# Kernel tuning notes

Measured on AMD Instinct MI355X. Metric: run time of the kernel, lower is better.

Reference implementation:

```python
import jax, jax.numpy as jnp
import numpy as np

B, S, D = 4, 4096, 256

def setup_inputs() -> dict:
    key = jax.random.key(0)
    ks = jax.random.split(key, 9)
    sc = 1.0 / np.sqrt(D)
    return {
        "v": jax.random.normal(ks[0], (B, S, D), jnp.float32),
        "k": jax.random.normal(ks[1], (B, S, D), jnp.float32),
        "q": jax.random.normal(ks[2], (B, S, D), jnp.float32),
        "Wq": jax.random.normal(ks[3], (D, D), jnp.float32) * sc,
        "bq": jnp.zeros((D,), jnp.float32),
        "Wk": jax.random.normal(ks[4], (D, D), jnp.float32) * sc,
        "bk": jnp.zeros((D,), jnp.float32),
        "Wv": jax.random.normal(ks[5], (D, D), jnp.float32) * sc,
        "bv": jnp.zeros((D,), jnp.float32),
    }

def reference(v, k, q, Wq, bq, Wk, bk, Wv, bv):
    d_model = q.shape[-1]
    seq_len = q.shape[-2]
    qp = q @ Wq + bq                      # [B,S,D]
    kp = k @ Wk + bk
    vp = v @ Wv + bv
    # scores [B,S,S], scaled then MULTIPLIED by lower-triangular mask (faithful to original)
    scores = jnp.einsum('bqd,bkd->bqk', qp, kp) / jnp.sqrt(jnp.float32(d_model))
    mask = jnp.tril(jnp.ones((seq_len, seq_len), scores.dtype))
    scores = scores * mask
    attn = jax.nn.softmax(scores, axis=-1)
    return qp + jnp.einsum('bqk,bkd->bqd', attn, vp)
```

## Files before the change

kernel.cpp:

```cpp
#include <hip/hip_runtime.h>
#include <hip/hip_bf16.h>


typedef __bf16 bf16x8 __attribute__((ext_vector_type(8)));
typedef float f32x4 __attribute__((ext_vector_type(4)));
typedef float f32x16 __attribute__((ext_vector_type(16)));
typedef unsigned int u32x4 __attribute__((ext_vector_type(4)));

#define MASKV -3.0e38f

__device__ __forceinline__ unsigned short f2bf_u(float f) {
  unsigned u = __float_as_uint(f);
  u += 0x7fffu + ((u >> 16) & 1u);
  return (unsigned short)(u >> 16);
}
__device__ __forceinline__ float bf2f(unsigned u16) {
  return __uint_as_float(u16 << 16);
}
__device__ __forceinline__ unsigned short cvt_bf(float f) {
  return __builtin_bit_cast(unsigned short, (__bf16)f);
}

__global__ __launch_bounds__(256) void wt_kernel(
    const float* __restrict__ Wq, const float* __restrict__ Wk, const float* __restrict__ Wv,
    unsigned short* __restrict__ WTq, unsigned short* __restrict__ WTk, unsigned short* __restrict__ WTv) {
  int j = blockIdx.x & 255;
  int wsel = blockIdx.x >> 8;
  const float* W = wsel == 0 ? Wq : (wsel == 1 ? Wk : Wv);
  unsigned short* WT = wsel == 0 ? WTq : (wsel == 1 ? WTk : WTv);
  int k = threadIdx.x;
  WT[j * 256 + k] = f2bf_u(W[k * 256 + j]);
}

__global__ __launch_bounds__(256) void proj_all_kernel(
    const float* __restrict__ q_in, const float* __restrict__ k_in, const float* __restrict__ v_in,
    const unsigned short* __restrict__ WTq, const unsigned short* __restrict__ WTk,
    const unsigned short* __restrict__ WTv,
    const float* __restrict__ bq, const float* __restrict__ bk, const float* __restrict__ bv,
    unsigned short* __restrict__ qpb, unsigned short* __restrict__ kpb,
    unsigned short* __restrict__ vptb) {
  int mode = blockIdx.y;
  const float* X = mode == 0 ? q_in : (mode == 1 ? k_in : v_in);
  const unsigned short* WT = mode == 0 ? WTq : (mode == 1 ? WTk : WTv);
  const float* bias = mode == 0 ? bq : (mode == 1 ? bk : bv);

  int rt = blockIdx.x;
  int tid = threadIdx.x;
  int w = tid >> 6, l = tid & 63, g = l >> 4, lm = l & 15;
  int arow = rt * 64 + w * 16 + lm;

  f32x4 acc[16];
#pragma unroll
  for (int i = 0; i < 16; i++) acc[i] = (f32x4){0.f, 0.f, 0.f, 0.f};

#pragma unroll
  for (int kb = 0; kb < 256; kb += 32) {
    const float* ap = X + arow * 256 + kb + 8 * g;
    float4 a0 = *(const float4*)ap;
    float4 a1 = *(const float4*)(ap + 4);
    bf16x8 af;
    af[0] = (__bf16)a0.x; af[1] = (__bf16)a0.y; af[2] = (__bf16)a0.z; af[3] = (__bf16)a0.w;
    af[4] = (__bf16)a1.x; af[5] = (__bf16)a1.y; af[6] = (__bf16)a1.z; af[7] = (__bf16)a1.w;
#pragma unroll
    for (int nt = 0; nt < 16; nt++) {
      bf16x8 bf = *(const bf16x8*)(WT + (nt * 16 + lm) * 256 + kb + 8 * g);
      acc[nt] = __builtin_amdgcn_mfma_f32_16x16x32_bf16(af, bf, acc[nt], 0, 0, 0);
    }
  }

#pragma unroll
  for (int nt = 0; nt < 16; nt++) {
    int col = nt * 16 + lm;
    float bb = bias[col];
#pragma unroll
    for (int r = 0; r < 4; r++) {
      int orow = rt * 64 + w * 16 + 4 * g + r;
      float v = acc[nt][r] + bb;
      int idx = orow * 256 + col;
      if (mode == 0) {
        qpb[idx] = f2bf_u(v * 0.0625f);
      } else if (mode == 1) {
        kpb[idx] = f2bf_u(v * 1.4426950408889634f);
      } else {
        int b = orow >> 12, sidx = orow & 4095;
        vptb[(((size_t)b * 128 + (sidx >> 5)) * 256 + col) * 32 + (sidx & 31)] = f2bf_u(v);
      }
    }
  }
}

__global__ __launch_bounds__(256) void scan1(const unsigned short* __restrict__ vptb,
                                             float* __restrict__ ctot) {
  int c = blockIdx.x, b = blockIdx.y, d = threadIdx.x;
  const unsigned short* base = vptb + (((size_t)b * 128 + c) * 256 + d) * 32;
  float acc = 0.f;
#pragma unroll
  for (int r = 0; r < 32; r++) acc += bf2f(base[r]);
  ctot[(b * 128 + c) * 256 + d] = acc;
}

__global__ __launch_bounds__(256) void scan2(const unsigned short* __restrict__ vptb,
                                             const float* __restrict__ ctot,
                                             unsigned short* __restrict__ suffv) {
  int c = blockIdx.x, b = blockIdx.y, d = threadIdx.x;
  float acc = 0.f;
  for (int c2 = c + 1; c2 < 128; c2++) acc += ctot[(b * 128 + c2) * 256 + d];
  const unsigned short* base = vptb + (((size_t)b * 128 + c) * 256 + d) * 32;
  unsigned short* sbase = suffv + ((size_t)b * 4096 + c * 32) * 256 + d;
  for (int r = 31; r >= 0; r--) {
    sbase[r * 256] = f2bf_u(acc);
    acc += bf2f(base[r]);
  }
}

__global__ __launch_bounds__(256, 2) void attn13_kernel(
    const unsigned short* __restrict__ qpb, const unsigned short* __restrict__ kpb,
    const unsigned short* __restrict__ vptb,
    unsigned short* __restrict__ slot01,
    unsigned short* __restrict__ slot23,
    unsigned short* __restrict__ slot45,
    float* __restrict__ mz) {
  extern __shared__ char smem[];

  int bid = blockIdx.x;
  int low = bid & 7;
  int b = low >> 1, shi = low & 1;
  int j = bid >> 3;
  int jd3 = j / 3;
  int qb = 31 - jd3;
  int s = shi * 3 + (j - jd3 * 3);
  int NT = 4 * (qb + 1);
  int t0 = (s * NT) / 6, t1 = ((s + 1) * NT) / 6;

  int tid = threadIdx.x;
  int wv = tid >> 6, l = tid & 63;
  int hi = l >> 5, r32 = l & 31;
  int vsw = (r32 >> 1) & 3;
  int ksw = r32 & 7;

  int qwave = qb * 128 + 32 * wv;
  int qglob = qwave + r32;

  bf16x8 qf[16];
  const unsigned short* qsrc = qpb + (size_t)(b * 4096 + qwave + r32) * 256;
#pragma unroll
  for (int st = 0; st < 16; st++) qf[st] = *(const bf16x8*)(qsrc + st * 16 + 8 * hi);

  f32x16 zero16;
#pragma unroll
  for (int ee = 0; ee < 16; ee++) zero16[ee] = 0.f;
  f32x16 O[8];
#pragma unroll
  for (int dt = 0; dt < 8; dt++) O[dt] = zero16;
  float m_ = -1e30f, Z_ = 0.f;

  const unsigned short* kbase0 = kpb + (size_t)b * 4096 * 256;
  const unsigned short* vbase0 = vptb + (size_t)b * 128 * 256 * 32;

  auto STAGE = [&](int bi, int kt) {
    char* Kdst = smem + bi * 16384;
    char* Vdst = smem + 32768 + bi * 16384;
    const unsigned short* ksrc = kbase0 + (size_t)kt * 32 * 256;
    const unsigned short* vtile = vbase0 + (size_t)kt * 256 * 32;
#pragma unroll
    for (int j2 = 0; j2 < 4; j2++) {
      int ch = wv * 4 + j2;
      int row = ch * 2 + (l >> 5);
      int cc = (l & 31) ^ (row & 7);
      __builtin_amdgcn_global_load_lds(
          (const __attribute__((address_space(1))) unsigned int*)(ksrc + row * 256 + cc * 8),
          (__attribute__((address_space(3))) unsigned int*)(Kdst + ch * 1024), 16, 0, 0);
    }
#pragma unroll
    for (int j2 = 0; j2 < 4; j2++) {
      int ch = wv * 4 + j2;
      int d = ch * 16 + (l >> 2);
      int cc = (l & 3) ^ ((l >> 3) & 3);
      __builtin_amdgcn_global_load_lds(
          (const __attribute__((address_space(1))) unsigned int*)(vtile + d * 32 + cc * 8),
          (__attribute__((address_space(3))) unsigned int*)(Vdst + ch * 1024), 16, 0, 0);
    }
  };

  if (t0 < t1) {
    STAGE(0, t0);
    if (t0 + 1 < t1) STAGE(1, t0 + 1);
  }

  for (int kt = t0; kt < t1; kt++) {
    int cur = (kt - t0) & 1;
    int kb2 = kt * 32;

    if (kt + 1 < t1) asm volatile("s_waitcnt vmcnt(8)" ::: "memory");
    else             asm volatile("s_waitcnt vmcnt(0)" ::: "memory");
    __builtin_amdgcn_s_barrier();
    __builtin_amdgcn_sched_barrier(0);

    if (kb2 <= qwave + 31) {
      const char* Kp = smem + cur * 16384;
      const char* Vp = smem + 32768 + cur * 16384;

      f32x16 St;
      __builtin_amdgcn_s_setprio(1);
      {
        bf16x8 kf = *(const bf16x8*)(Kp + r32 * 512 + ((hi ^ ksw) * 16));
        St = __builtin_amdgcn_mfma_f32_32x32x16_bf16(kf, qf[0], zero16, 0, 0, 0);
      }
#pragma unroll
      for (int st = 1; st < 16; st++) {
        bf16x8 kf = *(const bf16x8*)(Kp + r32 * 512 + (((2 * st + hi) ^ ksw) * 16));
        St = __builtin_amdgcn_mfma_f32_32x32x16_bf16(kf, qf[st], St, 0, 0, 0);
      }
      __builtin_amdgcn_s_setprio(0);

      if (kb2 + 31 > qwave) {
#pragma unroll
        for (int r = 0; r < 16; r++) {
          int kg = kb2 + (r & 3) + 8 * (r >> 2) + 4 * hi;
          if (kg > qglob) St[r] = MASKV;
        }
      }

      float mx = fmaxf(fmaxf(fmaxf(St[0], St[1]), fmaxf(St[2], St[3])),
                       fmaxf(fmaxf(St[4], St[5]), fmaxf(St[6], St[7])));
      float mx2 = fmaxf(fmaxf(fmaxf(St[8], St[9]), fmaxf(St[10], St[11])),
                        fmaxf(fmaxf(St[12], St[13]), fmaxf(St[14], St[15])));
      mx = fmaxf(mx, mx2);
      mx = fmaxf(mx, __shfl_xor(mx, 32));
      bool upd = __any(mx > m_ + 8.f);
      if (upd) {
        float mn = fmaxf(m_, mx);
        float scl = exp2f(m_ - mn);
        m_ = mn;
        Z_ *= scl;
#pragma unroll
        for (int r = 0; r < 16; r++) {
          int qr = (r & 3) + 8 * (r >> 2) + 4 * hi;
          float sb = __uint_as_float(
              (unsigned)__builtin_amdgcn_ds_bpermute(qr * 4, (int)__float_as_uint(scl)));
#pragma unroll
          for (int dt = 0; dt < 8; dt++) O[dt][r] *= sb;
        }
      }
      float p[16];
#pragma unroll
      for (int r = 0; r < 16; r++) p[r] = exp2f(St[r] - m_);
      float rs = ((p[0] + p[1]) + (p[2] + p[3])) + ((p[4] + p[5]) + (p[6] + p[7])) +
                 (((p[8] + p[9]) + (p[10] + p[11])) + ((p[12] + p[13]) + (p[14] + p[15])));
      rs += __shfl_xor(rs, 32);
      Z_ += rs;

      unsigned X[8];
#pragma unroll
      for (int i = 0; i < 8; i++)
        X[i] = (unsigned)cvt_bf(p[2 * i]) | ((unsigned)cvt_bf(p[2 * i + 1]) << 16);
      unsigned Y0 = (unsigned)__shfl_xor((int)X[0], 32);
      unsigned Y1 = (unsigned)__shfl_xor((int)X[1], 32);
      unsigned Y2 = (unsigned)__shfl_xor((int)X[2], 32);
      unsigned Y3 = (unsigned)__shfl_xor((int)X[3], 32);
      unsigned Y4 = (unsigned)__shfl_xor((int)X[4], 32);
      unsigned Y5 = (unsigned)__shfl_xor((int)X[5], 32);
      unsigned Y6 = (unsigned)__shfl_xor((int)X[6], 32);
      unsigned Y7 = (unsigned)__shfl_xor((int)X[7], 32);
      u32x4 A0, A1;
      A0[0] = hi ? Y2 : X[0]; A0[1] = hi ? Y3 : X[1];
      A0[2] = hi ? X[2] : Y0; A0[3] = hi ? X[3] : Y1;
      A1[0] = hi ? Y6 : X[4]; A1[1] = hi ? Y7 : X[5];
      A1[2] = hi ? X[6] : Y4; A1[3] = hi ? X[7] : Y5;
      bf16x8 pa0 = __builtin_bit_cast(bf16x8, A0);
      bf16x8 pa1 = __builtin_bit_cast(bf16x8, A1);

      __builtin_amdgcn_s_setprio(1);
#pragma unroll
      for (int dt = 0; dt < 8; dt++) {
        bf16x8 vf0 = *(const bf16x8*)(Vp + (dt * 32 + r32) * 64 + ((hi ^ vsw) * 16));
        O[dt] = __builtin_amdgcn_mfma_f32_32x32x16_bf16(pa0, vf0, O[dt], 0, 0, 0);
      }
#pragma unroll
      for (int dt = 0; dt < 8; dt++) {
        bf16x8 vf1 = *(const bf16x8*)(Vp + (dt * 32 + r32) * 64 + (((2 + hi) ^ vsw) * 16));
        O[dt] = __builtin_amdgcn_mfma_f32_32x32x16_bf16(pa1, vf1, O[dt], 0, 0, 0);
      }
      __builtin_amdgcn_s_setprio(0);
    }

    __builtin_amdgcn_sched_barrier(0);
    __builtin_amdgcn_s_barrier();
    if (kt + 2 < t1) STAGE(cur, kt + 2);
  }

  int grow_base = b * 4096 + qwave;
  if (hi == 0) {
    float* mzm = mz + s * 32768;
    mzm[grow_base + r32] = m_;
    mzm[16384 + grow_base + r32] = Z_;
  }
#pragma unroll
  for (int r = 0; r < 16; r++) {
    int qr = (r & 3) + 8 * (r >> 2) + 4 * hi;
    size_t grow = (size_t)(grow_base + qr);
#pragma unroll
    for (int dt = 0; dt < 8; dt++) {
      int dcol = dt * 32 + r32;
      unsigned short vb = cvt_bf(O[dt][r]);
      if (s < 2)
        slot01[grow * 512 + (size_t)s * 256 + dcol] = vb;
      else if (s < 4)
        slot23[(size_t)(s - 2) * 4194304 + grow * 256 + dcol] = vb;
      else
        slot45[(size_t)(s - 4) * 4194304 + grow * 256 + dcol] = vb;
    }
  }
}

__global__ __launch_bounds__(256) void combine6_kernel(
    const float* __restrict__ mz,
    const unsigned short* __restrict__ slot23, const unsigned short* __restrict__ slot45,
    const unsigned short* __restrict__ qpb, const unsigned short* __restrict__ suffv,
    float* __restrict__ out) {
  int grow = blockIdx.x * 4 + (threadIdx.x >> 6);
  int col = (threadIdx.x & 63) * 4;
  const unsigned short* slot01 = (const unsigned short*)out;

  float mv[6], Zv[6];
#pragma unroll
  for (int s = 0; s < 6; s++) {
    const float* mzm = mz + s * 32768;
    mv[s] = mzm[grow];
    Zv[s] = mzm[16384 + grow];
  }
  float M = mv[0];
#pragma unroll
  for (int s = 1; s < 6; s++) M = fmaxf(M, mv[s]);
  float fs[6], Zm = 0.f;
#pragma unroll
  for (int s = 0; s < 6; s++) {
    fs[s] = exp2f(mv[s] - M);
    Zm += Zv[s] * fs[s];
  }

  int q = grow & 4095;
  int nmask = 4095 - q;
  float scl, e0, Zf;
  if (nmask > 0) {
    float Mf = fmaxf(M, 0.f);
    scl = exp2f(M - Mf);
    e0 = exp2f(-Mf);
    Zf = Zm * scl + (float)nmask * e0;
  } else {
    scl = 1.f; e0 = 0.f; Zf = Zm;
  }
  float rZ = 1.f / Zf;
  float a[6];
#pragma unroll
  for (int s = 0; s < 6; s++) a[s] = fs[s] * scl * rZ;
  float asv = e0 * rZ;

  size_t base = (size_t)grow * 256 + col;
  uint2 ss[6];
  ss[0] = *(const uint2*)(slot01 + (size_t)grow * 512 + col);
  ss[1] = *(const uint2*)(slot01 + (size_t)grow * 512 + 256 + col);
  ss[2] = *(const uint2*)(slot23 + base);
  ss[3] = *(const uint2*)(slot23 + 4194304 + base);
  ss[4] = *(const uint2*)(slot45 + base);
  ss[5] = *(const uint2*)(slot45 + 4194304 + base);
  uint2 qpr = *(const uint2*)(qpb + base);
  uint2 svu = *(const uint2*)(suffv + base);

  __syncthreads();

  float4 res;
  res.x = 16.f * bf2f(qpr.x & 0xffff) + bf2f(svu.x & 0xffff) * asv;
  res.y = 16.f * bf2f(qpr.x >> 16) + bf2f(svu.x >> 16) * asv;
  res.z = 16.f * bf2f(qpr.y & 0xffff) + bf2f(svu.y & 0xffff) * asv;
  res.w = 16.f * bf2f(qpr.y >> 16) + bf2f(svu.y >> 16) * asv;
#pragma unroll
  for (int s = 0; s < 6; s++) {
    res.x += bf2f(ss[s].x & 0xffff) * a[s];
    res.y += bf2f(ss[s].x >> 16) * a[s];
    res.z += bf2f(ss[s].y & 0xffff) * a[s];
    res.w += bf2f(ss[s].y >> 16) * a[s];
  }
  *(float4*)&out[base] = res;
}

extern "C" void kernel_launch(void* const* d_in, const int* in_sizes, int n_in,
                              void* d_out, int out_size, void* d_ws, size_t ws_size,
                              hipStream_t stream) {
  const float* v_in = (const float*)d_in[0];
  const float* k_in = (const float*)d_in[1];
  const float* q_in = (const float*)d_in[2];
  const float* Wq = (const float*)d_in[3];
  const float* bq = (const float*)d_in[4];
  const float* Wk = (const float*)d_in[5];
  const float* bk = (const float*)d_in[6];
  const float* Wv = (const float*)d_in[7];
  const float* bv = (const float*)d_in[8];
  float* out = (float*)d_out;

  char* p = (char*)d_ws;
  unsigned short* slot45 = (unsigned short*)(p + 0);
  unsigned short* slot23 = (unsigned short*)(p + 16777216);
  unsigned short* suffv = (unsigned short*)(p + 33554432);
  unsigned short* qpb = (unsigned short*)(p + 41943040);
  unsigned short* kpb = (unsigned short*)(p + 50331648);
  unsigned short* vptb = (unsigned short*)(p + 58720256);
  float* mz = (float*)(p + 67108864);
  unsigned short* WTq = (unsigned short*)(p + 67895296);
  unsigned short* WTk = (unsigned short*)(p + 68026368);
  unsigned short* WTv = (unsigned short*)(p + 68157440);
  float* ctot = (float*)(p + 68288512);
  unsigned short* slot01 = (unsigned short*)d_out;

  hipFuncSetAttribute((const void*)attn13_kernel,
                      hipFuncAttributeMaxDynamicSharedMemorySize, 65536);

  wt_kernel<<<768, 256, 0, stream>>>(Wq, Wk, Wv, WTq, WTk, WTv);
  proj_all_kernel<<<dim3(256, 3), 256, 0, stream>>>(q_in, k_in, v_in, WTq, WTk, WTv,
                                                    bq, bk, bv, qpb, kpb, vptb);
  scan1<<<dim3(128, 4), 256, 0, stream>>>(vptb, ctot);
  scan2<<<dim3(128, 4), 256, 0, stream>>>(vptb, ctot, suffv);
  attn13_kernel<<<768, 256, 65536, stream>>>(qpb, kpb, vptb, slot01, slot23, slot45, mz);
  combine6_kernel<<<4096, 256, 0, stream>>>(mz, slot23, slot45, qpb, suffv, out);
}
```

Before: 187.3 us.

## Stage projection weight tiles into LDS with async double-buffered global_load_lds

The projection GEMM used to read bf16 weight fragments straight from global memory inside the MFMA loop. It now copies each 32-wide K slice of the transposed weights into a double-buffered 32KB shared-memory region using global_load_lds, with an XOR swizzle to avoid bank conflicts. vmcnt waits and barriers overlap the next slice's load with the current MFMAs. This adds block-wide barriers and LDS use per block, and the projection is only a small part of the total pipeline. The attention kernel is only renamed.

Measured after the change: 151.8 us. 18.9% less time.

```diff
diff --git a/kernel.cpp b/kernel.cpp
--- a/kernel.cpp
+++ b/kernel.cpp
@@ -39,6 +39,8 @@
     const float* __restrict__ bq, const float* __restrict__ bk, const float* __restrict__ bv,
     unsigned short* __restrict__ qpb, unsigned short* __restrict__ kpb,
     unsigned short* __restrict__ vptb) {
+  __shared__ char bsmem[32768];
+
   int mode = blockIdx.y;
   const float* X = mode == 0 ? q_in : (mode == 1 ? k_in : v_in);
   const unsigned short* WT = mode == 0 ? WTq : (mode == 1 ? WTk : WTv);
@@ -48,24 +50,56 @@
   int tid = threadIdx.x;
   int w = tid >> 6, l = tid & 63, g = l >> 4, lm = l & 15;
   int arow = rt * 64 + w * 16 + lm;
+  int lsw = lm & 3;
 
   f32x4 acc[16];
 #pragma unroll
   for (int i = 0; i < 16; i++) acc[i] = (f32x4){0.f, 0.f, 0.f, 0.f};
 
-#pragma unroll
-  for (int kb = 0; kb < 256; kb += 32) {
+  auto BSTAGE = [&](int bi, int kb) {
+    char* dstbase = bsmem + bi * 16384 + w * 1024;
+#pragma unroll
+    for (int i = 0; i < 4; i++) {
+      int chunkid = i * 256 + w * 64 + l;
+      int col = chunkid >> 2, cc = chunkid & 3;
+      const unsigned short* src = WT + col * 256 + kb + 8 * (cc ^ (col & 3));
+      __builtin_amdgcn_global_load_lds(
+          (const __attribute__((address_space(1))) unsigned int*)src,
+          (__attribute__((address_space(3))) unsigned int*)(dstbase + i * 4096), 16, 0, 0);
+    }
+  };
+
+  BSTAGE(0, 0);
+  BSTAGE(1, 32);
+
+  for (int kb8 = 0; kb8 < 8; kb8++) {
+    int cur = kb8 & 1;
+    int kb = kb8 * 32;
+
+    if (kb8 + 1 < 8) asm volatile("s_waitcnt vmcnt(4)" ::: "memory");
+    else             asm volatile("s_waitcnt vmcnt(0)" ::: "memory");
+    __builtin_amdgcn_s_barrier();
+    __builtin_amdgcn_sched_barrier(0);
+
     const float* ap = X + arow * 256 + kb + 8 * g;
     float4 a0 = *(const float4*)ap;
     float4 a1 = *(const float4*)(ap + 4);
     bf16x8 af;
     af[0] = (__bf16)a0.x; af[1] = (__bf16)a0.y; af[2] = (__bf16)a0.z; af[3] = (__bf16)a0.w;
     af[4] = (__bf16)a1.x; af[5] = (__bf16)a1.y; af[6] = (__bf16)a1.z; af[7] = (__bf16)a1.w;
+
+    const char* Bs = bsmem + cur * 16384;
+    __builtin_amdgcn_s_setprio(1);
 #pragma unroll
     for (int nt = 0; nt < 16; nt++) {
-      bf16x8 bf = *(const bf16x8*)(WT + (nt * 16 + lm) * 256 + kb + 8 * g);
+      bf16x8 bf = *(const bf16x8*)(Bs + (nt * 16 + lm) * 64 + ((g ^ lsw) * 16));
       acc[nt] = __builtin_amdgcn_mfma_f32_16x16x32_bf16(af, bf, acc[nt], 0, 0, 0);
     }
+    __builtin_amdgcn_s_setprio(0);
+
+    __builtin_amdgcn_sched_barrier(0);
+    __builtin_amdgcn_s_barrier();
+    if (kb8 + 2 < 8) BSTAGE(cur, kb + 64);
   }
 
 #pragma unroll
@@ -113,7 +147,7 @@
   }
 }
 
-__global__ __launch_bounds__(256, 2) void attn13_kernel(
+__global__ __launch_bounds__(256, 2) void attn14_kernel(
     const unsigned short* __restrict__ qpb, const unsigned short* __restrict__ kpb,
     const unsigned short* __restrict__ vptb,
     unsigned short* __restrict__ slot01,
@@ -412,7 +446,7 @@
   float* ctot = (float*)(p + 68288512);
   unsigned short* slot01 = (unsigned short*)d_out;
 
-  hipFuncSetAttribute((const void*)attn13_kernel,
+  hipFuncSetAttribute((const void*)attn14_kernel,
                       hipFuncAttributeMaxDynamicSharedMemorySize, 65536);
 
   wt_kernel<<<768, 256, 0, stream>>>(Wq, Wk, Wv, WTq, WTk, WTv);
@@ -420,6 +454,6 @@
                                                     bq, bk, bv, qpb, kpb, vptb);
   scan1<<<dim3(128, 4), 256, 0, stream>>>(vptb, ctot);
   scan2<<<dim3(128, 4), 256, 0, stream>>>(vptb, ctot, suffv);
-  attn13_kernel<<<768, 256, 65536, stream>>>(qpb, kpb, vptb, slot01, slot23, slot45, mz);
+  attn14_kernel<<<768, 256, 65536, stream>>>(qpb, kpb, vptb, slot01, slot23, slot45, mz);
   combine6_kernel<<<4096, 256, 0, stream>>>(mz, slot23, slot45, qpb, suffv, out);
 }
```
